# Kernel tuning notes

Measured on AMD Instinct MI355X. Metric: run time of the kernel, lower is better.

The kernel has to match this reference:

```python
import jax, jax.numpy as jnp
import numpy as np
from jax import lax

B, T, IN, H, OUT = 4096, 512, 2, 12, 2


def setup_inputs() -> dict:
    key = jax.random.key(0)
    ks = jax.random.split(key, 11)
    s = 1.0 / np.sqrt(H)  # PyTorch LSTM init scale
    f32 = jnp.float32
    return {
        "x": jax.random.normal(ks[0], (B, T, IN), dtype=f32),
        "W_ih0": jax.random.uniform(ks[1], (4 * H, IN), dtype=f32, minval=-s, maxval=s),
        "W_hh0": jax.random.uniform(ks[2], (4 * H, H), dtype=f32, minval=-s, maxval=s),
        "b_ih0": jax.random.uniform(ks[3], (4 * H,), dtype=f32, minval=-s, maxval=s),
        "b_hh0": jax.random.uniform(ks[4], (4 * H,), dtype=f32, minval=-s, maxval=s),
        "W_ih1": jax.random.uniform(ks[5], (4 * H, H), dtype=f32, minval=-s, maxval=s),
        "W_hh1": jax.random.uniform(ks[6], (4 * H, H), dtype=f32, minval=-s, maxval=s),
        "b_ih1": jax.random.uniform(ks[7], (4 * H,), dtype=f32, minval=-s, maxval=s),
        "b_hh1": jax.random.uniform(ks[8], (4 * H,), dtype=f32, minval=-s, maxval=s),
        "fc_W": jax.random.uniform(ks[9], (OUT, H), dtype=f32, minval=-s, maxval=s),
        "fc_b": jax.random.uniform(ks[10], (OUT,), dtype=f32, minval=-s, maxval=s),
    }


def _lstm_layer(x, W_ih, W_hh, b_ih, b_hh):
    # x: [B, T, in_dim] -> hidden trajectory [B, T, H]
    b, h = x.shape[0], W_hh.shape[1]
    # Precompute input contribution for all timesteps: [T, B, 4H]
    xg = jnp.einsum('bti,gi->tbg', x, W_ih) + b_ih + b_hh

    def step(carry, xg_t):
        hprev, cprev = carry
        gates = xg_t + hprev @ W_hh.T  # [B, 4H], PyTorch gate order i,f,g,o
        i, f, g, o = jnp.split(gates, 4, axis=-1)
        i = jax.nn.sigmoid(i)
        f = jax.nn.sigmoid(f)
        g = jnp.tanh(g)
        o = jax.nn.sigmoid(o)
        c = f * cprev + i * g
        hnew = o * jnp.tanh(c)
        return (hnew, c), hnew

    z = jnp.zeros((b, h), dtype=x.dtype)
    _, hs = lax.scan(step, (z, z), xg)  # hs: [T, B, H]
    return jnp.swapaxes(hs, 0, 1)  # [B, T, H]


def reference(x, W_ih0, W_hh0, b_ih0, b_hh0, W_ih1, W_hh1, b_ih1, b_hh1, fc_W, fc_b):
    # 2-layer LSTM, h0=c0=0; dropout is identity in eval mode.
    h1 = _lstm_layer(x, W_ih0, W_hh0, b_ih0, b_hh0)   # [B, T, H]
    h2 = _lstm_layer(h1, W_ih1, W_hh1, b_ih1, b_hh1)  # [B, T, H]
    last = h2[:, -1, :]                               # [B, H]
    return last @ fc_W.T + fc_b                       # [B, OUT]
```

## Files before the change

kernel.cpp:

```cpp
#include <hip/hip_runtime.h>


namespace {
constexpr int H  = 12;
constexpr int T  = 512;
constexpr float LOG2E = 1.4426950408889634f;

typedef float f2 __attribute__((ext_vector_type(2)));

__device__ __forceinline__ f2 fma2(f2 a, f2 b, f2 c) {
    return __builtin_elementwise_fma(a, b, c);
}
__device__ __forceinline__ float exp2_(float x) {
    float r; asm("v_exp_f32 %0, %1" : "=v"(r) : "v"(x)); return r;
}
__device__ __forceinline__ float rcp_(float x) { return __builtin_amdgcn_rcpf(x); }
__device__ __forceinline__ void memfence_() { asm volatile("" ::: "memory"); }

template <int CTRL>
__device__ __forceinline__ float dppf(float v) {
    return __int_as_float(__builtin_amdgcn_update_dpp(
        __float_as_int(v), __float_as_int(v), CTRL, 0xF, 0xF, true));
}
constexpr int BC0 = 0x00;
constexpr int BC1 = 0x55;
constexpr int BC2 = 0xAA;
constexpr int BC3 = 0xFF;

__device__ __forceinline__ float tanh_(float c) {
    return fmaf(2.0f, rcp_(1.0f + exp2_(-2.0f * LOG2E * c)), -1.0f);
}
}

__global__
__attribute__((amdgpu_flat_work_group_size(256, 256)))
__attribute__((amdgpu_waves_per_eu(4, 4)))
void lstm2_fc_kernel(
    const float* __restrict__ x,
    const float* __restrict__ W_ih0,
    const float* __restrict__ W_hh0,
    const float* __restrict__ b_ih0,
    const float* __restrict__ b_hh0,
    const float* __restrict__ W_ih1,
    const float* __restrict__ W_hh1,
    const float* __restrict__ b_ih1,
    const float* __restrict__ b_hh1,
    const float* __restrict__ fc_W,
    const float* __restrict__ fc_b,
    float* __restrict__ out)
{
    const int lane = threadIdx.x & 63;
    const int wid  = __builtin_amdgcn_readfirstlane((int)threadIdx.x >> 6);
    const int b    = blockIdx.x * 4 + wid;
    const int u    = lane >> 2;
    const int gate = lane & 3;
    const int uc   = (u < H) ? u : 0;
    const int r    = gate * H + uc;

    const float pre  = (gate == 2) ? 2.0f : 1.0f;
    const float kmul = -LOG2E * pre;
    const float pa   = 1.0f - pre;

    __shared__ __align__(16) float sm[4 * 32];
    float* smb = &sm[wid * 32];
    const bool isL1 = (gate == 1);
    const bool pub  = (gate <= 1) && (u < H);
    float* smw = smb + (isL1 ? 16 : 0) + uc;

    f2 wx, whh0p[6], wih1p[6], whh1p[6];
    wx.x = kmul * W_ih0[r * 2 + 0];
    wx.y = kmul * W_ih0[r * 2 + 1];
#pragma unroll
    for (int k = 0; k < 6; ++k) {
        whh0p[k].x = kmul * W_hh0[r * H + 2 * k];
        whh0p[k].y = kmul * W_hh0[r * H + 2 * k + 1];
        wih1p[k].x = kmul * W_ih1[r * H + 2 * k];
        wih1p[k].y = kmul * W_ih1[r * H + 2 * k + 1];
        whh1p[k].x = kmul * W_hh1[r * H + 2 * k];
        whh1p[k].y = kmul * W_hh1[r * H + 2 * k + 1];
    }
    f2 bias0p, bias1p;
    bias0p.x = kmul * (b_ih0[r] + b_hh0[r]); bias0p.y = 0.0f;
    bias1p.x = kmul * (b_ih1[r] + b_hh1[r]); bias1p.y = 0.0f;

    float c = 0.0f;
    float I1s = 0.0f, F1s = 0.0f, G1s = 0.0f, O1s = 0.0f;
    f2 hp0[6], hq1[6];
#pragma unroll
    for (int k = 0; k < 6; ++k) { hp0[k] = (f2)(0.0f); hq1[k] = (f2)(0.0f); }

    const float* xp = x + (size_t)b * T * 2;

    auto step = [&](float xv0, float xv1) {
        f2 xv; xv.x = xv0; xv.y = xv1;
        f2 cA = fma2(wx, xv, bias0p);
        cA = fma2(whh0p[0], hp0[0], cA);
        cA = fma2(whh0p[1], hp0[1], cA);
        f2 cB = whh0p[2] * hp0[2];
        cB = fma2(whh0p[3], hp0[3], cB);
        f2 cC = whh0p[4] * hp0[4];
        cC = fma2(whh0p[5], hp0[5], cC);
        cA = cA + cB + cC;
        const float s0 = fmaf(pre, rcp_(1.0f + exp2_(cA.x + cA.y)), pa);
        const float I0 = dppf<BC0>(s0);
        const float F0 = dppf<BC1>(s0);
        const float G0 = dppf<BC2>(s0);
        const float O0 = dppf<BC3>(s0);
        const float I = isL1 ? I1s : I0;
        const float F = isL1 ? F1s : F0;
        const float G = isL1 ? G1s : G0;
        const float O = isL1 ? O1s : O0;
        c = fmaf(F, c, I * G);
        const float hv = O * tanh_(c);
        if (pub) *smw = hv;
        memfence_();
#pragma unroll
        for (int k = 0; k < 6; ++k) hp0[k] = *(const f2*)(smb + 2 * k);
#pragma unroll
        for (int k = 0; k < 6; ++k) hq1[k] = *(const f2*)(smb + 16 + 2 * k);
        f2 dA = fma2(whh1p[0], hq1[0], bias1p);
        dA = fma2(wih1p[0], hp0[0], dA);
        dA = fma2(whh1p[1], hq1[1], dA);
        dA = fma2(wih1p[1], hp0[1], dA);
        f2 dB = whh1p[2] * hq1[2];
        dB = fma2(wih1p[2], hp0[2], dB);
        dB = fma2(whh1p[3], hq1[3], dB);
        dB = fma2(wih1p[3], hp0[3], dB);
        f2 dC = whh1p[4] * hq1[4];
        dC = fma2(wih1p[4], hp0[4], dC);
        dC = fma2(whh1p[5], hq1[5], dC);
        dC = fma2(wih1p[5], hp0[5], dC);
        dA = dA + dB + dC;
        const float s1 = fmaf(pre, rcp_(1.0f + exp2_(dA.x + dA.y)), pa);
        I1s = dppf<BC0>(s1);
        F1s = dppf<BC1>(s1);
        G1s = dppf<BC2>(s1);
        O1s = dppf<BC3>(s1);
    };

    float2 xc = *(const float2*)xp;
    for (int t = 0; t < T - 1; ++t) {
        const float2 xn = *(const float2*)(xp + 2 * (t + 1));
        step(xc.x, xc.y);
        xc = xn;
    }
    step(xc.x, xc.y);

    {
        const float cE = fmaf(F1s, c, I1s * G1s);
        const float hE = O1s * tanh_(cE);
        if (pub && isL1) *smw = hE;
        memfence_();
    }

    if (lane == 0) {
        float r0 = fc_b[0];
        float r1 = fc_b[1];
#pragma unroll
        for (int j = 0; j < H; ++j) {
            const float hj = smb[16 + j];
            r0 = fmaf(fc_W[j],     hj, r0);
            r1 = fmaf(fc_W[H + j], hj, r1);
        }
        float2 res; res.x = r0; res.y = r1;
        *(float2*)(out + (size_t)b * 2) = res;
    }
}

extern "C" void kernel_launch(void* const* d_in, const int* in_sizes, int n_in,
                              void* d_out, int out_size, void* d_ws, size_t ws_size,
                              hipStream_t stream) {
    const float* x     = (const float*)d_in[0];
    const float* W_ih0 = (const float*)d_in[1];
    const float* W_hh0 = (const float*)d_in[2];
    const float* b_ih0 = (const float*)d_in[3];
    const float* b_hh0 = (const float*)d_in[4];
    const float* W_ih1 = (const float*)d_in[5];
    const float* W_hh1 = (const float*)d_in[6];
    const float* b_ih1 = (const float*)d_in[7];
    const float* b_hh1 = (const float*)d_in[8];
    const float* fc_W  = (const float*)d_in[9];
    const float* fc_b  = (const float*)d_in[10];
    float* out = (float*)d_out;

    lstm2_fc_kernel<<<1024, 256, 0, stream>>>(
        x, W_ih0, W_hh0, b_ih0, b_hh0,
        W_ih1, W_hh1, b_ih1, b_hh1, fc_W, fc_b, out);
}
```

Before: 252.5 us.

## Serialize layer 0 and layer 1 per step, broadcasting h0 via ds_bpermute

The earlier kernel skewed the two layers by one timestep so each lane group ran layer 0 or layer 1 of the cell update at once, sharing results through LDS. The new loop computes layer 0's cell, broadcasts h0 to all lanes with twelve ds_bpermute ops, then computes layer 1 in the same step, issuing layer 1's recurrent-weight FMAs early to overlap the permute latency. Only h1 still goes through LDS. This removes the skew, the select logic and one LDS round trip. The cost is a longer serial dependency chain per step: two sigmoid/tanh stages plus the bpermute latency.

```diff
diff --git a/kernel.cpp b/kernel.cpp
--- a/kernel.cpp
+++ b/kernel.cpp
@@ -2,8 +2,8 @@
 
 
 namespace {
-constexpr int H  = 12;
-constexpr int T  = 512;
+constexpr int H = 12;
+constexpr int T = 512;
 constexpr float LOG2E = 1.4426950408889634f;
 
 typedef float f2 __attribute__((ext_vector_type(2)));
@@ -16,13 +16,15 @@
 }
 __device__ __forceinline__ float rcp_(float x) { return __builtin_amdgcn_rcpf(x); }
 __device__ __forceinline__ void memfence_() { asm volatile("" ::: "memory"); }
+__device__ __forceinline__ float bperm_(int addr, float v) {
+    return __int_as_float(__builtin_amdgcn_ds_bpermute(addr, __float_as_int(v)));
+}
 
 template <int CTRL>
 __device__ __forceinline__ float dppf(float v) {
     return __int_as_float(__builtin_amdgcn_update_dpp(
         __float_as_int(v), __float_as_int(v), CTRL, 0xF, 0xF, true));
 }
-constexpr int BC0 = 0x00;
 constexpr int BC1 = 0x55;
 constexpr int BC2 = 0xAA;
 constexpr int BC3 = 0xFF;
@@ -61,11 +63,10 @@
     const float kmul = -LOG2E * pre;
     const float pa   = 1.0f - pre;
 
-    __shared__ __align__(16) float sm[4 * 32];
-    float* smb = &sm[wid * 32];
-    const bool isL1 = (gate == 1);
-    const bool pub  = (gate <= 1) && (u < H);
-    float* smw = smb + (isL1 ? 16 : 0) + uc;
+    __shared__ float sm[4 * 16];
+    float* smb = &sm[wid * 16];
+    const bool writer = (gate == 0) && (u < H);
+    float* smw = smb + uc;
 
     f2 wx, whh0p[6], wih1p[6], whh1p[6];
     wx.x = kmul * W_ih0[r * 2 + 0];
@@ -83,84 +84,79 @@
     bias0p.x = kmul * (b_ih0[r] + b_hh0[r]); bias0p.y = 0.0f;
     bias1p.x = kmul * (b_ih1[r] + b_hh1[r]); bias1p.y = 0.0f;
 
-    float c = 0.0f;
-    float I1s = 0.0f, F1s = 0.0f, G1s = 0.0f, O1s = 0.0f;
-    f2 hp0[6], hq1[6];
+    float c0 = 0.0f, c1 = 0.0f;
+    f2 h0p[6], h1p[6];
 #pragma unroll
-    for (int k = 0; k < 6; ++k) { hp0[k] = (f2)(0.0f); hq1[k] = (f2)(0.0f); }
+    for (int k = 0; k < 6; ++k) { h0p[k] = (f2)(0.0f); h1p[k] = (f2)(0.0f); }
 
     const float* xp = x + (size_t)b * T * 2;
+    float2 xc = *(const float2*)xp;
 
-    auto step = [&](float xv0, float xv1) {
-        f2 xv; xv.x = xv0; xv.y = xv1;
+    for (int t = 0; t < T; ++t) {
+        const int tn = (t < T - 1) ? (t + 1) : t;
+        const float2 xn = *(const float2*)(xp + 2 * tn);
+
+        f2 xv; xv.x = xc.x; xv.y = xc.y;
         f2 cA = fma2(wx, xv, bias0p);
-        cA = fma2(whh0p[0], hp0[0], cA);
-        cA = fma2(whh0p[1], hp0[1], cA);
-        f2 cB = whh0p[2] * hp0[2];
-        cB = fma2(whh0p[3], hp0[3], cB);
-        f2 cC = whh0p[4] * hp0[4];
-        cC = fma2(whh0p[5], hp0[5], cC);
+        cA = fma2(whh0p[0], h0p[0], cA);
+        cA = fma2(whh0p[1], h0p[1], cA);
+        f2 cB = whh0p[2] * h0p[2];
+        cB = fma2(whh0p[3], h0p[3], cB);
+        f2 cC = whh0p[4] * h0p[4];
+        cC = fma2(whh0p[5], h0p[5], cC);
         cA = cA + cB + cC;
         const float s0 = fmaf(pre, rcp_(1.0f + exp2_(cA.x + cA.y)), pa);
-        const float I0 = dppf<BC0>(s0);
         const float F0 = dppf<BC1>(s0);
         const float G0 = dppf<BC2>(s0);
         const float O0 = dppf<BC3>(s0);
-        const float I = isL1 ? I1s : I0;
-        const float F = isL1 ? F1s : F0;
-        const float G = isL1 ? G1s : G0;
-        const float O = isL1 ? O1s : O0;
-        c = fmaf(F, c, I * G);
-        const float hv = O * tanh_(c);
-        if (pub) *smw = hv;
+        c0 = fmaf(F0, c0, s0 * G0);
+        const float h0v = O0 * tanh_(c0);
+
+        f2 dA = fma2(whh1p[0], h1p[0], bias1p);
+        dA = fma2(whh1p[1], h1p[1], dA);
+        f2 dB = whh1p[2] * h1p[2];
+        dB = fma2(whh1p[3], h1p[3], dB);
+        f2 dC = whh1p[4] * h1p[4];
+        dC = fma2(whh1p[5], h1p[5], dC);
+
+        h0p[0].x = bperm_(0,   h0v);  h0p[0].y = bperm_(16,  h0v);
+        h0p[1].x = bperm_(32,  h0v);  h0p[1].y = bperm_(48,  h0v);
+        h0p[2].x = bperm_(64,  h0v);  h0p[2].y = bperm_(80,  h0v);
+        h0p[3].x = bperm_(96,  h0v);  h0p[3].y = bperm_(112, h0v);
+        h0p[4].x = bperm_(128, h0v);  h0p[4].y = bperm_(144, h0v);
+        h0p[5].x = bperm_(160, h0v);  h0p[5].y = bperm_(176, h0v);
+
+        dA = fma2(wih1p[0], h0p[0], dA);
+        dA = fma2(wih1p[1], h0p[1], dA);
+        dB = fma2(wih1p[2], h0p[2], dB);
+        dB = fma2(wih1p[3], h0p[3], dB);
+        dC = fma2(wih1p[4], h0p[4], dC);
+        dC = fma2(wih1p[5], h0p[5], dC);
+        dA = dA + dB + dC;
+        const float s1 = fmaf(pre, rcp_(1.0f + exp2_(dA.x + dA.y)), pa);
+        const float F1 = dppf<BC1>(s1);
+        const float G1 = dppf<BC2>(s1);
+        const float O1 = dppf<BC3>(s1);
+        c1 = fmaf(F1, c1, s1 * G1);
+        const float h1v = O1 * tanh_(c1);
+
+        if (writer) *smw = h1v;
         memfence_();
 #pragma unroll
-        for (int k = 0; k < 6; ++k) hp0[k] = *(const f2*)(smb + 2 * k);
-#pragma unroll
-        for (int k = 0; k < 6; ++k) hq1[k] = *(const f2*)(smb + 16 + 2 * k);
-        f2 dA = fma2(whh1p[0], hq1[0], bias1p);
-        dA = fma2(wih1p[0], hp0[0], dA);
-        dA = fma2(whh1p[1], hq1[1], dA);
-        dA = fma2(wih1p[1], hp0[1], dA);
-        f2 dB = whh1p[2] * hq1[2];
-        dB = fma2(wih1p[2], hp0[2], dB);
-        dB = fma2(whh1p[3], hq1[3], dB);
-        dB = fma2(wih1p[3], hp0[3], dB);
-        f2 dC = whh1p[4] * hq1[4];
-        dC = fma2(wih1p[4], hp0[4], dC);
-        dC = fma2(whh1p[5], hq1[5], dC);
-        dC = fma2(wih1p[5], hp0[5], dC);
-        dA = dA + dB + dC;
-        const float s1 = fmaf(pre, rcp_(1.0f + exp2_(dA.x + dA.y)), pa);
-        I1s = dppf<BC0>(s1);
-        F1s = dppf<BC1>(s1);
-        G1s = dppf<BC2>(s1);
-        O1s = dppf<BC3>(s1);
-    };
+        for (int k = 0; k < 6; ++k) h1p[k] = *(const f2*)(smb + 2 * k);
 
-    float2 xc = *(const float2*)xp;
-    for (int t = 0; t < T - 1; ++t) {
-        const float2 xn = *(const float2*)(xp + 2 * (t + 1));
-        step(xc.x, xc.y);
         xc = xn;
-    }
-    step(xc.x, xc.y);
-
-    {
-        const float cE = fmaf(F1s, c, I1s * G1s);
-        const float hE = O1s * tanh_(cE);
-        if (pub && isL1) *smw = hE;
-        memfence_();
     }
 
     if (lane == 0) {
         float r0 = fc_b[0];
         float r1 = fc_b[1];
 #pragma unroll
-        for (int j = 0; j < H; ++j) {
-            const float hj = smb[16 + j];
-            r0 = fmaf(fc_W[j],     hj, r0);
-            r1 = fmaf(fc_W[H + j], hj, r1);
+        for (int k = 0; k < 6; ++k) {
+            r0 = fmaf(fc_W[2 * k],     h1p[k].x, r0);
+            r0 = fmaf(fc_W[2 * k + 1], h1p[k].y, r0);
+            r1 = fmaf(fc_W[H + 2 * k],     h1p[k].x, r1);
+            r1 = fmaf(fc_W[H + 2 * k + 1], h1p[k].y, r1);
         }
         float2 res; res.x = r0; res.y = r1;
         *(float2*)(out + (size_t)b * 2) = res;
```

After: 330.4 us. 30.9% more time.
